# Kernel optimization log

Measured on AMD Instinct MI355X. Metric: run time of the kernel, lower is better.

The kernel has to match this reference:

```python
import jax, jax.numpy as jnp
import numpy as np

N, E, D, H, L, G, C = 50000, 800000, 128, 128, 3, 128, 10
BN_EPS = 1e-5


def setup_inputs() -> dict:
    key = jax.random.key(0)
    ks = jax.random.split(key, 16)
    inp = {
        "x": jax.random.normal(ks[0], (N, D), dtype=jnp.float32),
        "node_centrality": jax.random.uniform(ks[1], (N,), dtype=jnp.float32),
        "edge_centrality": jax.random.uniform(ks[2], (E,), dtype=jnp.float32),
        # stacked per-layer MLP params (in == hidden so stackable)
        "W1": jax.random.normal(ks[3], (L, D, H), dtype=jnp.float32) * 0.05,
        "b1": jnp.zeros((L, H), dtype=jnp.float32),
        "g1": jnp.ones((L, H), dtype=jnp.float32),
        "be1": jnp.zeros((L, H), dtype=jnp.float32),
        "W2": jax.random.normal(ks[4], (L, H, H), dtype=jnp.float32) * 0.05,
        "b2": jnp.zeros((L, H), dtype=jnp.float32),
        "Wc": jax.random.normal(ks[5], (H, C), dtype=jnp.float32) * 0.05,
        "bc": jnp.zeros((C,), dtype=jnp.float32),
        "edge_index": jax.random.randint(ks[6], (2, E), 0, N, dtype=jnp.int64),
        "batch": jnp.sort(jax.random.randint(ks[7], (N,), 0, G, dtype=jnp.int64)),
    }
    return inp


def _gin_forward(x, node_centrality, edge_centrality, W1, b1, g1, be1, W2, b2, Wc, bc, edge_index, batch):
    src, dst = edge_index[0], edge_index[1]  # x_j = x[src], aggregate at dst
    ec = edge_centrality[:, None]
    nc = node_centrality[:, None]
    for l in range(L):
        # message: gather + scale by edge centrality; aggr='add': scatter-add
        msg = x[src] * ec                                      # [E, H]
        agg = jax.ops.segment_sum(msg, dst, num_segments=N)    # [N, H]
        h = agg * nc + x                                       # (1 + eps) * x_r, eps = 0
        # MLP([in, hidden, hidden]): Linear -> BatchNorm(train) -> ReLU -> Linear
        h = h @ W1[l] + b1[l]
        mu = h.mean(axis=0)
        var = h.var(axis=0)  # biased, matches BN training stats
        h = (h - mu) * jax.lax.rsqrt(var + BN_EPS) * g1[l] + be1[l]
        h = jax.nn.relu(h)
        h = h @ W2[l] + b2[l]
        x = jax.nn.relu(h)  # outer .relu() in GIN.forward
    # global mean pool over graphs
    sums = jax.ops.segment_sum(x, batch, num_segments=G)           # [G, H]
    cnt = jax.ops.segment_sum(jnp.ones((N,), x.dtype), batch, num_segments=G)
    pooled = sums / jnp.maximum(cnt, 1.0)[:, None]
    return pooled @ Wc + bc  # [G, C]


def reference(x, edge_index, batch, node_centrality, edge_centrality, W1, b1, g1, be1, W2, b2, Wc, bc):
    return _gin_forward(x, node_centrality, edge_centrality, W1, b1, g1, be1, W2, b2, Wc, bc, edge_index, batch)
```

## Files before the change

### kernel.cpp

```cpp
#include <hip/hip_runtime.h>

#define Nn 50000
#define Ee 800000
#define HD 128
#define Ll 3
#define Gg 128
#define Cc 10
#define BN_EPS 1e-5f
#define NBLK1 782
#define PPAD 800
#define NSCB 49

__global__ void k_deg(const int* __restrict__ dst, int* __restrict__ deg) {
  int i = blockIdx.x * blockDim.x + threadIdx.x;
  int stride = gridDim.x * blockDim.x;
  for (int e = i; e < Ee; e += stride) atomicAdd(&deg[dst[e]], 1);
}

__global__ void k_scan1(const int* __restrict__ deg, int* __restrict__ offs,
                        int* __restrict__ bsum) {
  __shared__ int b0[1024], b1[1024];
  int tid = threadIdx.x;
  int i = blockIdx.x * 1024 + tid;
  int v = (i < Nn) ? deg[i] : 0;
  int* cur = b0; int* nxt = b1;
  cur[tid] = v;
  __syncthreads();
  for (int off = 1; off < 1024; off <<= 1) {
    int s = cur[tid] + ((tid >= off) ? cur[tid - off] : 0);
    nxt[tid] = s;
    __syncthreads();
    int* t = cur; cur = nxt; nxt = t;
  }
  if (i < Nn) offs[i] = cur[tid] - v;
  if (tid == 1023) bsum[blockIdx.x] = cur[1023];
}

__global__ void k_scan2(const int* __restrict__ bsum, int* __restrict__ carry) {
  int lane = threadIdx.x;
  int v = (lane < NSCB) ? bsum[lane] : 0;
  int s = v;
  for (int off = 1; off < 64; off <<= 1) {
    int t = __shfl_up(s, off, 64);
    if (lane >= off) s += t;
  }
  if (lane < NSCB) carry[lane] = s - v;
}

__global__ void k_scan3(const int* __restrict__ carry, int* __restrict__ offs,
                        int* __restrict__ cursor) {
  int i = blockIdx.x * 1024 + threadIdx.x;
  if (i < Nn) {
    int o = offs[i] + carry[blockIdx.x];
    offs[i] = o; cursor[i] = o;
  }
  if (i == 0) offs[Nn] = Ee;
}

__global__ void k_fill(const int* __restrict__ src, const int* __restrict__ dst,
                       const float* __restrict__ ec, int* __restrict__ cursor,
                       int* __restrict__ esrc, float* __restrict__ ew) {
  int i = blockIdx.x * blockDim.x + threadIdx.x;
  int stride = gridDim.x * blockDim.x;
  for (int e = i; e < Ee; e += stride) {
    int d = dst[e];
    int p = atomicAdd(&cursor[d], 1);
    esrc[p] = src[e];
    ew[p]   = ec[e];
  }
}

__global__ void k_agg(const float* __restrict__ xin, const int* __restrict__ offs,
                      const int* __restrict__ esrc, const float* __restrict__ ew,
                      float* __restrict__ agg) {
  int wid = threadIdx.x >> 6, lane = threadIdx.x & 63;
  int n = blockIdx.x * 4 + wid;
  if (n >= Nn) return;
  int beg = offs[n], end = offs[n + 1];
  const float2* x2 = (const float2*)xin;
  float2 acc0 = make_float2(0.f, 0.f);
  float2 acc1 = make_float2(0.f, 0.f);
  int j = beg;
  for (; j + 1 < end; j += 2) {
    int s0 = esrc[j], s1 = esrc[j + 1];
    float w0 = ew[j], w1 = ew[j + 1];
    float2 v0 = x2[s0 * 64 + lane];
    float2 v1 = x2[s1 * 64 + lane];
    acc0.x = fmaf(v0.x, w0, acc0.x); acc0.y = fmaf(v0.y, w0, acc0.y);
    acc1.x = fmaf(v1.x, w1, acc1.x); acc1.y = fmaf(v1.y, w1, acc1.y);
  }
  if (j < end) {
    int s0 = esrc[j];
    float w0 = ew[j];
    float2 v0 = x2[s0 * 64 + lane];
    acc0.x = fmaf(v0.x, w0, acc0.x); acc0.y = fmaf(v0.y, w0, acc0.y);
  }
  acc0.x += acc1.x; acc0.y += acc1.y;
  ((float2*)agg)[n * 64 + lane] = acc0;
}

__launch_bounds__(256, 2)
__global__ void k_gemm1(const float* __restrict__ agg, const float* __restrict__ nc,
                        const float* __restrict__ xin, const float* __restrict__ W,
                        const float* __restrict__ bias, float* __restrict__ out,
                        float* __restrict__ partial) {
  __shared__ float Als[64][132];
  __shared__ float4 Wls[64 * 32];
  int tid = threadIdx.x;
  int row0 = blockIdx.x * 64;

  int c4 = tid & 31, rr = tid >> 5;
  for (int it = 0; it < 8; ++it) {
    int r = rr + it * 8;
    int grow = row0 + r;
    float4 a = make_float4(0.f, 0.f, 0.f, 0.f);
    if (grow < Nn) {
      float4 ag = ((const float4*)agg)[grow * 32 + c4];
      float4 xv = ((const float4*)xin)[grow * 32 + c4];
      float nv = nc[grow];
      a.x = fmaf(ag.x, nv, xv.x); a.y = fmaf(ag.y, nv, xv.y);
      a.z = fmaf(ag.z, nv, xv.z); a.w = fmaf(ag.w, nv, xv.w);
    }
    *(float4*)&Als[r][c4 * 4] = a;
  }

  int tx = tid & 31, ty = tid >> 5;
  float acc[8][4];
#pragma unroll
  for (int i = 0; i < 8; ++i)
#pragma unroll
    for (int j = 0; j < 4; ++j) acc[i][j] = 0.f;

  for (int h = 0; h < 2; ++h) {
    if (h) __syncthreads();
    const float4* Wf4 = (const float4*)(W + h * 64 * 128);
    for (int i = tid; i < 2048; i += 256) Wls[i] = Wf4[i];
    __syncthreads();

#pragma unroll 4
    for (int kk = 0; kk < 64; kk += 4) {
      float4 b0 = Wls[(kk + 0) * 32 + tx];
      float4 b1v = Wls[(kk + 1) * 32 + tx];
      float4 b2v = Wls[(kk + 2) * 32 + tx];
      float4 b3v = Wls[(kk + 3) * 32 + tx];
#pragma unroll
      for (int i = 0; i < 8; ++i) {
        float4 av = *(const float4*)&Als[ty * 8 + i][h * 64 + kk];
        acc[i][0] = fmaf(av.x, b0.x, acc[i][0]); acc[i][1] = fmaf(av.x, b0.y, acc[i][1]);
        acc[i][2] = fmaf(av.x, b0.z, acc[i][2]); acc[i][3] = fmaf(av.x, b0.w, acc[i][3]);
        acc[i][0] = fmaf(av.y, b1v.x, acc[i][0]); acc[i][1] = fmaf(av.y, b1v.y, acc[i][1]);
        acc[i][2] = fmaf(av.y, b1v.z, acc[i][2]); acc[i][3] = fmaf(av.y, b1v.w, acc[i][3]);
        acc[i][0] = fmaf(av.z, b2v.x, acc[i][0]); acc[i][1] = fmaf(av.z, b2v.y, acc[i][1]);
        acc[i][2] = fmaf(av.z, b2v.z, acc[i][2]); acc[i][3] = fmaf(av.z, b2v.w, acc[i][3]);
        acc[i][0] = fmaf(av.w, b3v.x, acc[i][0]); acc[i][1] = fmaf(av.w, b3v.y, acc[i][1]);
        acc[i][2] = fmaf(av.w, b3v.z, acc[i][2]); acc[i][3] = fmaf(av.w, b3v.w, acc[i][3]);
      }
    }
  }

  float4 bcol = ((const float4*)bias)[tx];
  float s0 = 0, s1 = 0, s2 = 0, s3 = 0, q0 = 0, q1 = 0, q2 = 0, q3 = 0;
#pragma unroll
  for (int i = 0; i < 8; ++i) {
    int grow = row0 + ty * 8 + i;
    if (grow < Nn) {
      float4 o;
      o.x = acc[i][0] + bcol.x; o.y = acc[i][1] + bcol.y;
      o.z = acc[i][2] + bcol.z; o.w = acc[i][3] + bcol.w;
      ((float4*)out)[grow * 32 + tx] = o;
      s0 += o.x; s1 += o.y; s2 += o.z; s3 += o.w;
      q0 += o.x * o.x; q1 += o.y * o.y; q2 += o.z * o.z; q3 += o.w * o.w;
    }
  }

  __syncthreads();
  float* red = (float*)Als;
  red[tid * 8 + 0] = s0; red[tid * 8 + 1] = s1;
  red[tid * 8 + 2] = s2; red[tid * 8 + 3] = s3;
  red[tid * 8 + 4] = q0; red[tid * 8 + 5] = q1;
  red[tid * 8 + 6] = q2; red[tid * 8 + 7] = q3;
  __syncthreads();
  if (ty == 0) {
    float v[8];
#pragma unroll
    for (int j = 0; j < 8; ++j) v[j] = 0.f;
    for (int t = 0; t < 8; ++t) {
      int id = t * 32 + tx;
#pragma unroll
      for (int j = 0; j < 8; ++j) v[j] += red[id * 8 + j];
    }
    int blk = blockIdx.x;
#pragma unroll
    for (int j = 0; j < 4; ++j) {
      partial[(tx * 4 + j) * PPAD + blk]         = v[j];
      partial[(128 + tx * 4 + j) * PPAD + blk]   = v[4 + j];
    }
  }
}

__global__ void k_bnfin(const float* __restrict__ partial,
                        const float* __restrict__ g1, const float* __restrict__ be1,
                        float* __restrict__ scaleA, float* __restrict__ shiftA) {
  __shared__ float ss[256], qq[256];
  int f = blockIdx.x, t = threadIdx.x;
  float s = 0.f, q = 0.f;
  for (int b = t; b < NBLK1; b += 256) {
    s += partial[f * PPAD + b];
    q += partial[(128 + f) * PPAD + b];
  }
  ss[t] = s; qq[t] = q;
  __syncthreads();
  for (int off = 128; off > 0; off >>= 1) {
    if (t < off) { ss[t] += ss[t + off]; qq[t] += qq[t + off]; }
    __syncthreads();
  }
  if (t == 0) {
    const float inv = 1.0f / (float)Nn;
    float mu = ss[0] * inv;
    float var = fmaxf(qq[0] * inv - mu * mu, 0.f);
    float rs = rsqrtf(var + BN_EPS);
    float sc = rs * g1[f];
    scaleA[f] = sc;
    shiftA[f] = be1[f] - mu * sc;
  }
}

__launch_bounds__(256, 2)
__global__ void k_gemm2(const float* __restrict__ h1, const float* __restrict__ scaleA,
                        const float* __restrict__ shiftA, const float* __restrict__ W,
                        const float* __restrict__ bias, float* __restrict__ out) {
  __shared__ float Als[64][132];
  __shared__ float4 Wls[64 * 32];
  int tid = threadIdx.x;
  int row0 = blockIdx.x * 64;

  int c4 = tid & 31, rr = tid >> 5;
  float4 sc = ((const float4*)scaleA)[c4];
  float4 sh = ((const float4*)shiftA)[c4];
  for (int it = 0; it < 8; ++it) {
    int r = rr + it * 8;
    int grow = row0 + r;
    float4 a = make_float4(0.f, 0.f, 0.f, 0.f);
    if (grow < Nn) {
      float4 h = ((const float4*)h1)[grow * 32 + c4];
      a.x = fmaxf(fmaf(h.x, sc.x, sh.x), 0.f);
      a.y = fmaxf(fmaf(h.y, sc.y, sh.y), 0.f);
      a.z = fmaxf(fmaf(h.z, sc.z, sh.z), 0.f);
      a.w = fmaxf(fmaf(h.w, sc.w, sh.w), 0.f);
    }
    *(float4*)&Als[r][c4 * 4] = a;
  }

  int tx = tid & 31, ty = tid >> 5;
  float acc[8][4];
#pragma unroll
  for (int i = 0; i < 8; ++i)
#pragma unroll
    for (int j = 0; j < 4; ++j) acc[i][j] = 0.f;

  for (int h = 0; h < 2; ++h) {
    if (h) __syncthreads();
    const float4* Wf4 = (const float4*)(W + h * 64 * 128);
    for (int i = tid; i < 2048; i += 256) Wls[i] = Wf4[i];
    __syncthreads();

#pragma unroll 4
    for (int kk = 0; kk < 64; kk += 4) {
      float4 b0 = Wls[(kk + 0) * 32 + tx];
      float4 b1v = Wls[(kk + 1) * 32 + tx];
      float4 b2v = Wls[(kk + 2) * 32 + tx];
      float4 b3v = Wls[(kk + 3) * 32 + tx];
#pragma unroll
      for (int i = 0; i < 8; ++i) {
        float4 av = *(const float4*)&Als[ty * 8 + i][h * 64 + kk];
        acc[i][0] = fmaf(av.x, b0.x, acc[i][0]); acc[i][1] = fmaf(av.x, b0.y, acc[i][1]);
        acc[i][2] = fmaf(av.x, b0.z, acc[i][2]); acc[i][3] = fmaf(av.x, b0.w, acc[i][3]);
        acc[i][0] = fmaf(av.y, b1v.x, acc[i][0]); acc[i][1] = fmaf(av.y, b1v.y, acc[i][1]);
        acc[i][2] = fmaf(av.y, b1v.z, acc[i][2]); acc[i][3] = fmaf(av.y, b1v.w, acc[i][3]);
        acc[i][0] = fmaf(av.z, b2v.x, acc[i][0]); acc[i][1] = fmaf(av.z, b2v.y, acc[i][1]);
        acc[i][2] = fmaf(av.z, b2v.z, acc[i][2]); acc[i][3] = fmaf(av.z, b2v.w, acc[i][3]);
        acc[i][0] = fmaf(av.w, b3v.x, acc[i][0]); acc[i][1] = fmaf(av.w, b3v.y, acc[i][1]);
        acc[i][2] = fmaf(av.w, b3v.z, acc[i][2]); acc[i][3] = fmaf(av.w, b3v.w, acc[i][3]);
      }
    }
  }

  float4 bcol = ((const float4*)bias)[tx];
#pragma unroll
  for (int i = 0; i < 8; ++i) {
    int grow = row0 + ty * 8 + i;
    if (grow < Nn) {
      float4 o;
      o.x = fmaxf(acc[i][0] + bcol.x, 0.f);
      o.y = fmaxf(acc[i][1] + bcol.y, 0.f);
      o.z = fmaxf(acc[i][2] + bcol.z, 0.f);
      o.w = fmaxf(acc[i][3] + bcol.w, 0.f);
      ((float4*)out)[grow * 32 + tx] = o;
    }
  }
}

#define PCH 64
__global__ void k_pool(const float* __restrict__ xin, const int* __restrict__ batch,
                       float* __restrict__ pooled, float* __restrict__ gcnt) {
  int wid = threadIdx.x >> 6, lane = threadIdx.x & 63;
  int w = blockIdx.x * 4 + wid;
  int n0 = w * PCH;
  if (n0 >= Nn) return;
  int n1 = (n0 + PCH < Nn) ? n0 + PCH : Nn;
  const float2* x2 = (const float2*)xin;
  float2 acc = make_float2(0.f, 0.f);
  int cur = batch[n0];
  int cnt = 0;
  for (int n = n0; n < n1; ++n) {
    int g = batch[n];
    if (g != cur) {
      atomicAdd(&pooled[cur * 128 + lane * 2 + 0], acc.x);
      atomicAdd(&pooled[cur * 128 + lane * 2 + 1], acc.y);
      if (lane == 0) atomicAdd(&gcnt[cur], (float)cnt);
      acc = make_float2(0.f, 0.f); cnt = 0; cur = g;
    }
    float2 v = x2[n * 64 + lane];
    acc.x += v.x; acc.y += v.y; ++cnt;
  }
  atomicAdd(&pooled[cur * 128 + lane * 2 + 0], acc.x);
  atomicAdd(&pooled[cur * 128 + lane * 2 + 1], acc.y);
  if (lane == 0) atomicAdd(&gcnt[cur], (float)cnt);
}

__global__ void k_head(const float* __restrict__ pooled, const float* __restrict__ gcnt,
                       const float* __restrict__ Wc, const float* __restrict__ bc,
                       float* __restrict__ out) {
  __shared__ float p[128];
  int g = blockIdx.x, tid = threadIdx.x;
  p[tid] = pooled[g * 128 + tid] / fmaxf(gcnt[g], 1.0f);
  __syncthreads();
  if (tid < Cc) {
    float acc = bc[tid];
    for (int k = 0; k < 128; ++k) acc = fmaf(p[k], Wc[k * Cc + tid], acc);
    out[g * Cc + tid] = acc;
  }
}

extern "C" void kernel_launch(void* const* d_in, const int* in_sizes, int n_in,
                              void* d_out, int out_size, void* d_ws, size_t ws_size,
                              hipStream_t stream) {
  const float* x    = (const float*)d_in[0];
  const float* ncn  = (const float*)d_in[1];
  const float* ecn  = (const float*)d_in[2];
  const float* W1   = (const float*)d_in[3];
  const float* b1   = (const float*)d_in[4];
  const float* g1   = (const float*)d_in[5];
  const float* be1  = (const float*)d_in[6];
  const float* W2   = (const float*)d_in[7];
  const float* b2   = (const float*)d_in[8];
  const float* Wc   = (const float*)d_in[9];
  const float* bc   = (const float*)d_in[10];
  const int*   ei   = (const int*)d_in[11];
  const int*   batch= (const int*)d_in[12];
  const int* src  = ei;
  const int* dstp = ei + Ee;

  float* fws = (float*)d_ws;
  float* bufA     = fws;
  float* bufB     = fws +  6400000;
  float* h1       = fws + 12800000;
  float* partial  = fws + 19200000;
  float* scaleA   = partial + 256 * PPAD;
  float* shiftA   = scaleA + 128;
  float* pooled   = shiftA + 128;
  float* gcnt     = pooled + Gg * 128;
  int*   deg      = (int*)(gcnt + 128);
  int*   offs     = deg + Nn;
  int*   cursor   = offs + Nn + 64;
  int*   esrc     = cursor + Nn;
  float* ew       = (float*)(esrc + Ee);
  int*   bsum     = (int*)(ew + Ee);
  int*   carry    = bsum + 64;

  hipMemsetAsync(deg, 0, Nn * sizeof(int), stream);
  k_deg<<<1024, 256, 0, stream>>>(dstp, deg);
  k_scan1<<<NSCB, 1024, 0, stream>>>(deg, offs, bsum);
  k_scan2<<<1, 64, 0, stream>>>(bsum, carry);
  k_scan3<<<NSCB, 1024, 0, stream>>>(carry, offs, cursor);
  k_fill<<<1024, 256, 0, stream>>>(src, dstp, ecn, cursor, esrc, ew);

  const float* xin = x;
  for (int l = 0; l < Ll; ++l) {
    float* aggb = (l & 1) ? bufB : bufA;
    k_agg<<<(Nn + 3) / 4, 256, 0, stream>>>(xin, offs, esrc, ew, aggb);
    k_gemm1<<<NBLK1, 256, 0, stream>>>(aggb, ncn, xin, W1 + l * 128 * 128,
                                       b1 + l * 128, h1, partial);
    k_bnfin<<<128, 256, 0, stream>>>(partial, g1 + l * 128, be1 + l * 128,
                                     scaleA, shiftA);
    k_gemm2<<<NBLK1, 256, 0, stream>>>(h1, scaleA, shiftA, W2 + l * 128 * 128,
                                       b2 + l * 128, aggb);
    xin = aggb;
  }

  hipMemsetAsync(pooled, 0, (Gg * 128 + 128) * sizeof(float), stream);
  k_pool<<<(Nn + PCH * 4 - 1) / (PCH * 4), 256, 0, stream>>>(xin, batch, pooled, gcnt);
  k_head<<<Gg, 128, 0, stream>>>(pooled, gcnt, Wc, bc, (float*)d_out);
}
```

Measured before the change: 649.6 us.

## Use split-bf16 MFMA for the MLP GEMMs and pack the edge CSR arrays

Replaces the FP32 FMA shared-memory GEMMs with MFMA 16x16x32 bf16 instructions. Activations and weights are split into hi/lo bf16 pairs and three MFMAs are summed to recover near-FP32 accuracy. A new prep kernel transposes and splits W1/W2 once per call. Edge source and weight are packed into one int2 array, and the aggregation loop is unrolled to four edges to raise memory-level parallelism. The GEMMs now load A directly from global memory without LDS and use 128-thread blocks, which trades LDS reuse for MFMA throughput and adds a small approximation error.

```diff
diff --git a/kernel.cpp b/kernel.cpp
--- a/kernel.cpp
+++ b/kernel.cpp
@@ -10,6 +10,9 @@
 #define NBLK1 782
 #define PPAD 800
 #define NSCB 49
+
+typedef __attribute__((ext_vector_type(8))) __bf16 bf16x8;
+typedef __attribute__((ext_vector_type(4))) float f32x4;
 
 __global__ void k_deg(const int* __restrict__ dst, int* __restrict__ deg) {
   int i = blockIdx.x * blockDim.x + threadIdx.x;
@@ -59,141 +62,175 @@
 
 __global__ void k_fill(const int* __restrict__ src, const int* __restrict__ dst,
                        const float* __restrict__ ec, int* __restrict__ cursor,
-                       int* __restrict__ esrc, float* __restrict__ ew) {
+                       int2* __restrict__ epk) {
   int i = blockIdx.x * blockDim.x + threadIdx.x;
   int stride = gridDim.x * blockDim.x;
   for (int e = i; e < Ee; e += stride) {
     int d = dst[e];
     int p = atomicAdd(&cursor[d], 1);
-    esrc[p] = src[e];
-    ew[p]   = ec[e];
+    epk[p] = make_int2(src[e], __float_as_int(ec[e]));
+  }
+}
+
+__global__ void k_wprep(const float* __restrict__ W1, const float* __restrict__ W2,
+                        __bf16* __restrict__ wtHi, __bf16* __restrict__ wtLo) {
+  int mat = blockIdx.x >> 3;
+  int chunk = blockIdx.x & 7;
+  const float* W = (mat < 3) ? (W1 + mat * 16384) : (W2 + (mat - 3) * 16384);
+  __bf16* hi = wtHi + mat * 16384;
+  __bf16* lo = wtLo + mat * 16384;
+  for (int t = threadIdx.x; t < 2048; t += blockDim.x) {
+    int idx = chunk * 2048 + t;
+    int n = idx >> 7, k = idx & 127;
+    float v = W[k * 128 + n];
+    __bf16 h = (__bf16)v;
+    hi[idx] = h;
+    lo[idx] = (__bf16)(v - (float)h);
   }
 }
 
 __global__ void k_agg(const float* __restrict__ xin, const int* __restrict__ offs,
-                      const int* __restrict__ esrc, const float* __restrict__ ew,
-                      float* __restrict__ agg) {
+                      const int2* __restrict__ epk, float* __restrict__ agg) {
   int wid = threadIdx.x >> 6, lane = threadIdx.x & 63;
   int n = blockIdx.x * 4 + wid;
   if (n >= Nn) return;
   int beg = offs[n], end = offs[n + 1];
   const float2* x2 = (const float2*)xin;
-  float2 acc0 = make_float2(0.f, 0.f);
-  float2 acc1 = make_float2(0.f, 0.f);
+  float2 a0 = make_float2(0.f, 0.f), a1 = make_float2(0.f, 0.f);
+  float2 a2 = make_float2(0.f, 0.f), a3 = make_float2(0.f, 0.f);
   int j = beg;
-  for (; j + 1 < end; j += 2) {
-    int s0 = esrc[j], s1 = esrc[j + 1];
-    float w0 = ew[j], w1 = ew[j + 1];
-    float2 v0 = x2[s0 * 64 + lane];
-    float2 v1 = x2[s1 * 64 + lane];
-    acc0.x = fmaf(v0.x, w0, acc0.x); acc0.y = fmaf(v0.y, w0, acc0.y);
-    acc1.x = fmaf(v1.x, w1, acc1.x); acc1.y = fmaf(v1.y, w1, acc1.y);
-  }
-  if (j < end) {
-    int s0 = esrc[j];
-    float w0 = ew[j];
-    float2 v0 = x2[s0 * 64 + lane];
-    acc0.x = fmaf(v0.x, w0, acc0.x); acc0.y = fmaf(v0.y, w0, acc0.y);
-  }
-  acc0.x += acc1.x; acc0.y += acc1.y;
-  ((float2*)agg)[n * 64 + lane] = acc0;
-}
-
-__launch_bounds__(256, 2)
+  for (; j + 3 < end; j += 4) {
+    int2 e0 = epk[j], e1 = epk[j + 1], e2 = epk[j + 2], e3 = epk[j + 3];
+    float2 v0 = x2[e0.x * 64 + lane];
+    float2 v1 = x2[e1.x * 64 + lane];
+    float2 v2 = x2[e2.x * 64 + lane];
+    float2 v3 = x2[e3.x * 64 + lane];
+    float w0 = __int_as_float(e0.y), w1 = __int_as_float(e1.y);
+    float w2 = __int_as_float(e2.y), w3 = __int_as_float(e3.y);
+    a0.x = fmaf(v0.x, w0, a0.x); a0.y = fmaf(v0.y, w0, a0.y);
+    a1.x = fmaf(v1.x, w1, a1.x); a1.y = fmaf(v1.y, w1, a1.y);
+    a2.x = fmaf(v2.x, w2, a2.x); a2.y = fmaf(v2.y, w2, a2.y);
+    a3.x = fmaf(v3.x, w3, a3.x); a3.y = fmaf(v3.y, w3, a3.y);
+  }
+  for (; j < end; ++j) {
+    int2 e = epk[j];
+    float2 v = x2[e.x * 64 + lane];
+    float w = __int_as_float(e.y);
+    a0.x = fmaf(v.x, w, a0.x); a0.y = fmaf(v.y, w, a0.y);
+  }
+  a0.x += a1.x + a2.x + a3.x;
+  a0.y += a1.y + a2.y + a3.y;
+  ((float2*)agg)[n * 64 + lane] = a0;
+}
+
+__device__ __forceinline__ void split8(const float* a, bf16x8& hi, bf16x8& lo) {
+#pragma unroll
+  for (int j = 0; j < 8; ++j) {
+    float v = a[j];
+    __bf16 h = (__bf16)v;
+    hi[j] = h;
+    lo[j] = (__bf16)(v - (float)h);
+  }
+}
+
+__launch_bounds__(128)
 __global__ void k_gemm1(const float* __restrict__ agg, const float* __restrict__ nc,
-                        const float* __restrict__ xin, const float* __restrict__ W,
+                        const float* __restrict__ xin,
+                        const __bf16* __restrict__ wtHi, const __bf16* __restrict__ wtLo,
                         const float* __restrict__ bias, float* __restrict__ out,
                         float* __restrict__ partial) {
-  __shared__ float Als[64][132];
-  __shared__ float4 Wls[64 * 32];
   int tid = threadIdx.x;
+  int w = tid >> 6, l = tid & 63;
   int row0 = blockIdx.x * 64;
-
-  int c4 = tid & 31, rr = tid >> 5;
-  for (int it = 0; it < 8; ++it) {
-    int r = rr + it * 8;
-    int grow = row0 + r;
-    float4 a = make_float4(0.f, 0.f, 0.f, 0.f);
-    if (grow < Nn) {
-      float4 ag = ((const float4*)agg)[grow * 32 + c4];
-      float4 xv = ((const float4*)xin)[grow * 32 + c4];
-      float nv = nc[grow];
-      a.x = fmaf(ag.x, nv, xv.x); a.y = fmaf(ag.y, nv, xv.y);
-      a.z = fmaf(ag.z, nv, xv.z); a.w = fmaf(ag.w, nv, xv.w);
-    }
-    *(float4*)&Als[r][c4 * 4] = a;
-  }
-
-  int tx = tid & 31, ty = tid >> 5;
-  float acc[8][4];
-#pragma unroll
-  for (int i = 0; i < 8; ++i)
-#pragma unroll
-    for (int j = 0; j < 4; ++j) acc[i][j] = 0.f;
-
-  for (int h = 0; h < 2; ++h) {
-    if (h) __syncthreads();
-    const float4* Wf4 = (const float4*)(W + h * 64 * 128);
-    for (int i = tid; i < 2048; i += 256) Wls[i] = Wf4[i];
-    __syncthreads();
-
-#pragma unroll 4
-    for (int kk = 0; kk < 64; kk += 4) {
-      float4 b0 = Wls[(kk + 0) * 32 + tx];
-      float4 b1v = Wls[(kk + 1) * 32 + tx];
-      float4 b2v = Wls[(kk + 2) * 32 + tx];
-      float4 b3v = Wls[(kk + 3) * 32 + tx];
-#pragma unroll
-      for (int i = 0; i < 8; ++i) {
-        float4 av = *(const float4*)&Als[ty * 8 + i][h * 64 + kk];
-        acc[i][0] = fmaf(av.x, b0.x, acc[i][0]); acc[i][1] = fmaf(av.x, b0.y, acc[i][1]);
-        acc[i][2] = fmaf(av.x, b0.z, acc[i][2]); acc[i][3] = fmaf(av.x, b0.w, acc[i][3]);
-        acc[i][0] = fmaf(av.y, b1v.x, acc[i][0]); acc[i][1] = fmaf(av.y, b1v.y, acc[i][1]);
-        acc[i][2] = fmaf(av.y, b1v.z, acc[i][2]); acc[i][3] = fmaf(av.y, b1v.w, acc[i][3]);
-        acc[i][0] = fmaf(av.z, b2v.x, acc[i][0]); acc[i][1] = fmaf(av.z, b2v.y, acc[i][1]);
-        acc[i][2] = fmaf(av.z, b2v.z, acc[i][2]); acc[i][3] = fmaf(av.z, b2v.w, acc[i][3]);
-        acc[i][0] = fmaf(av.w, b3v.x, acc[i][0]); acc[i][1] = fmaf(av.w, b3v.y, acc[i][1]);
-        acc[i][2] = fmaf(av.w, b3v.z, acc[i][2]); acc[i][3] = fmaf(av.w, b3v.w, acc[i][3]);
-      }
-    }
-  }
-
-  float4 bcol = ((const float4*)bias)[tx];
-  float s0 = 0, s1 = 0, s2 = 0, s3 = 0, q0 = 0, q1 = 0, q2 = 0, q3 = 0;
-#pragma unroll
-  for (int i = 0; i < 8; ++i) {
-    int grow = row0 + ty * 8 + i;
-    if (grow < Nn) {
-      float4 o;
-      o.x = acc[i][0] + bcol.x; o.y = acc[i][1] + bcol.y;
-      o.z = acc[i][2] + bcol.z; o.w = acc[i][3] + bcol.w;
-      ((float4*)out)[grow * 32 + tx] = o;
-      s0 += o.x; s1 += o.y; s2 += o.z; s3 += o.w;
-      q0 += o.x * o.x; q1 += o.y * o.y; q2 += o.z * o.z; q3 += o.w * o.w;
-    }
-  }
-
-  __syncthreads();
-  float* red = (float*)Als;
-  red[tid * 8 + 0] = s0; red[tid * 8 + 1] = s1;
-  red[tid * 8 + 2] = s2; red[tid * 8 + 3] = s3;
-  red[tid * 8 + 4] = q0; red[tid * 8 + 5] = q1;
-  red[tid * 8 + 6] = q2; red[tid * 8 + 7] = q3;
-  __syncthreads();
-  if (ty == 0) {
-    float v[8];
-#pragma unroll
-    for (int j = 0; j < 8; ++j) v[j] = 0.f;
-    for (int t = 0; t < 8; ++t) {
-      int id = t * 32 + tx;
-#pragma unroll
-      for (int j = 0; j < 8; ++j) v[j] += red[id * 8 + j];
-    }
+  int l15 = l & 15, lg = l >> 4;
+  int colw = w * 64;
+  int krow = lg * 8;
+
+  f32x4 acc[4][4];
+#pragma unroll
+  for (int m = 0; m < 4; ++m)
+#pragma unroll
+    for (int n = 0; n < 4; ++n) acc[m][n] = (f32x4){0.f, 0.f, 0.f, 0.f};
+
+  int rowA[4]; bool rv[4]; float ncv[4];
+#pragma unroll
+  for (int m = 0; m < 4; ++m) {
+    rowA[m] = row0 + m * 16 + l15;
+    rv[m] = rowA[m] < Nn;
+    ncv[m] = rv[m] ? nc[rowA[m]] : 0.f;
+  }
+
+#pragma unroll
+  for (int ks = 0; ks < 4; ++ks) {
+    int k0 = ks * 32 + krow;
+    bf16x8 aHi[4], aLo[4];
+#pragma unroll
+    for (int m = 0; m < 4; ++m) {
+      float av[8];
+      if (rv[m]) {
+        const float* ap = agg + rowA[m] * 128 + k0;
+        const float* xp = xin + rowA[m] * 128 + k0;
+        f32x4 g0 = *(const f32x4*)ap, g1 = *(const f32x4*)(ap + 4);
+        f32x4 x0 = *(const f32x4*)xp, x1 = *(const f32x4*)(xp + 4);
+#pragma unroll
+        for (int jj = 0; jj < 4; ++jj) {
+          av[jj]     = fmaf(g0[jj], ncv[m], x0[jj]);
+          av[4 + jj] = fmaf(g1[jj], ncv[m], x1[jj]);
+        }
+      } else {
+#pragma unroll
+        for (int jj = 0; jj < 8; ++jj) av[jj] = 0.f;
+      }
+      split8(av, aHi[m], aLo[m]);
+    }
+    bf16x8 bHi[4], bLo[4];
+#pragma unroll
+    for (int n = 0; n < 4; ++n) {
+      int c = colw + n * 16 + l15;
+      bHi[n] = *(const bf16x8*)(wtHi + c * 128 + k0);
+      bLo[n] = *(const bf16x8*)(wtLo + c * 128 + k0);
+    }
+#pragma unroll
+    for (int m = 0; m < 4; ++m)
+#pragma unroll
+      for (int n = 0; n < 4; ++n) {
+        acc[m][n] = __builtin_amdgcn_mfma_f32_16x16x32_bf16(aHi[m], bHi[n], acc[m][n], 0, 0, 0);
+        acc[m][n] = __builtin_amdgcn_mfma_f32_16x16x32_bf16(aLo[m], bHi[n], acc[m][n], 0, 0, 0);
+        acc[m][n] = __builtin_amdgcn_mfma_f32_16x16x32_bf16(aHi[m], bLo[n], acc[m][n], 0, 0, 0);
+      }
+  }
+
+  float s[4] = {0.f, 0.f, 0.f, 0.f}, q[4] = {0.f, 0.f, 0.f, 0.f};
+#pragma unroll
+  for (int n = 0; n < 4; ++n) {
+    int c = colw + n * 16 + l15;
+    float bv = bias[c];
+#pragma unroll
+    for (int m = 0; m < 4; ++m) {
+      int rbase = row0 + m * 16 + lg * 4;
+#pragma unroll
+      for (int r = 0; r < 4; ++r) {
+        int rr = rbase + r;
+        if (rr < Nn) {
+          float o = acc[m][n][r] + bv;
+          out[rr * 128 + c] = o;
+          s[n] += o; q[n] += o * o;
+        }
+      }
+    }
+  }
+#pragma unroll
+  for (int n = 0; n < 4; ++n) {
+    s[n] += __shfl_xor(s[n], 16, 64); q[n] += __shfl_xor(q[n], 16, 64);
+    s[n] += __shfl_xor(s[n], 32, 64); q[n] += __shfl_xor(q[n], 32, 64);
+  }
+  if (lg == 0) {
     int blk = blockIdx.x;
 #pragma unroll
-    for (int j = 0; j < 4; ++j) {
-      partial[(tx * 4 + j) * PPAD + blk]         = v[j];
-      partial[(128 + tx * 4 + j) * PPAD + blk]   = v[4 + j];
+    for (int n = 0; n < 4; ++n) {
+      int f = colw + n * 16 + l15;
+      partial[f * PPAD + blk] = s[n];
+      partial[(128 + f) * PPAD + blk] = q[n];
     }
   }
 }
@@ -225,77 +262,83 @@
   }
 }
 
-__launch_bounds__(256, 2)
+__launch_bounds__(128)
 __global__ void k_gemm2(const float* __restrict__ h1, const float* __restrict__ scaleA,
-                        const float* __restrict__ shiftA, const float* __restrict__ W,
+                        const float* __restrict__ shiftA,
+                        const __bf16* __restrict__ wtHi, const __bf16* __restrict__ wtLo,
                         const float* __restrict__ bias, float* __restrict__ out) {
-  __shared__ float Als[64][132];
-  __shared__ float4 Wls[64 * 32];
   int tid = threadIdx.x;
+  int w = tid >> 6, l = tid & 63;
   int row0 = blockIdx.x * 64;
-
-  int c4 = tid & 31, rr = tid >> 5;
-  float4 sc = ((const float4*)scaleA)[c4];
-  float4 sh = ((const float4*)shiftA)[c4];
-  for (int it = 0; it < 8; ++it) {
-    int r = rr + it * 8;
-    int grow = row0 + r;
-    float4 a = make_float4(0.f, 0.f, 0.f, 0.f);
-    if (grow < Nn) {
-      float4 h = ((const float4*)h1)[grow * 32 + c4];
-      a.x = fmaxf(fmaf(h.x, sc.x, sh.x), 0.f);
-      a.y = fmaxf(fmaf(h.y, sc.y, sh.y), 0.f);
-      a.z = fmaxf(fmaf(h.z, sc.z, sh.z), 0.f);
-      a.w = fmaxf(fmaf(h.w, sc.w, sh.w), 0.f);
-    }
-    *(float4*)&Als[r][c4 * 4] = a;
-  }
-
-  int tx = tid & 31, ty = tid >> 5;
-  float acc[8][4];
-#pragma unroll
-  for (int i = 0; i < 8; ++i)
-#pragma unroll
-    for (int j = 0; j < 4; ++j) acc[i][j] = 0.f;
-
-  for (int h = 0; h < 2; ++h) {
-    if (h) __syncthreads();
-    const float4* Wf4 = (const float4*)(W + h * 64 * 128);
-    for (int i = tid; i < 2048; i += 256) Wls[i] = Wf4[i];
-    __syncthreads();
-
-#pragma unroll 4
-    for (int kk = 0; kk < 64; kk += 4) {
-      float4 b0 = Wls[(kk + 0) * 32 + tx];
-      float4 b1v = Wls[(kk + 1) * 32 + tx];
-      float4 b2v = Wls[(kk + 2) * 32 + tx];
-      float4 b3v = Wls[(kk + 3) * 32 + tx];
-#pragma unroll
-      for (int i = 0; i < 8; ++i) {
-        float4 av = *(const float4*)&Als[ty * 8 + i][h * 64 + kk];
-        acc[i][0] = fmaf(av.x, b0.x, acc[i][0]); acc[i][1] = fmaf(av.x, b0.y, acc[i][1]);
-        acc[i][2] = fmaf(av.x, b0.z, acc[i][2]); acc[i][3] = fmaf(av.x, b0.w, acc[i][3]);
-        acc[i][0] = fmaf(av.y, b1v.x, acc[i][0]); acc[i][1] = fmaf(av.y, b1v.y, acc[i][1]);
-        acc[i][2] = fmaf(av.y, b1v.z, acc[i][2]); acc[i][3] = fmaf(av.y, b1v.w, acc[i][3]);
-        acc[i][0] = fmaf(av.z, b2v.x, acc[i][0]); acc[i][1] = fmaf(av.z, b2v.y, acc[i][1]);
-        acc[i][2] = fmaf(av.z, b2v.z, acc[i][2]); acc[i][3] = fmaf(av.z, b2v.w, acc[i][3]);
-        acc[i][0] = fmaf(av.w, b3v.x, acc[i][0]); acc[i][1] = fmaf(av.w, b3v.y, acc[i][1]);
-        acc[i][2] = fmaf(av.w, b3v.z, acc[i][2]); acc[i][3] = fmaf(av.w, b3v.w, acc[i][3]);
-      }
-    }
-  }
-
-  float4 bcol = ((const float4*)bias)[tx];
-#pragma unroll
-  for (int i = 0; i < 8; ++i) {
-    int grow = row0 + ty * 8 + i;
-    if (grow < Nn) {
-      float4 o;
-      o.x = fmaxf(acc[i][0] + bcol.x, 0.f);
-      o.y = fmaxf(acc[i][1] + bcol.y, 0.f);
-      o.z = fmaxf(acc[i][2] + bcol.z, 0.f);
-      o.w = fmaxf(acc[i][3] + bcol.w, 0.f);
-      ((float4*)out)[grow * 32 + tx] = o;
+  int l15 = l & 15, lg = l >> 4;
+  int colw = w * 64;
+  int krow = lg * 8;
+
+  f32x4 acc[4][4];
+#pragma unroll
+  for (int m = 0; m < 4; ++m)
+#pragma unroll
+    for (int n = 0; n < 4; ++n) acc[m][n] = (f32x4){0.f, 0.f, 0.f, 0.f};
+
+  int rowA[4]; bool rv[4];
+#pragma unroll
+  for (int m = 0; m < 4; ++m) {
+    rowA[m] = row0 + m * 16 + l15;
+    rv[m] = rowA[m] < Nn;
+  }
+
+#pragma unroll
+  for (int ks = 0; ks < 4; ++ks) {
+    int k0 = ks * 32 + krow;
+    f32x4 sc0 = *(const f32x4*)(scaleA + k0), sc1 = *(const f32x4*)(scaleA + k0 + 4);
+    f32x4 sh0 = *(const f32x4*)(shiftA + k0), sh1 = *(const f32x4*)(shiftA + k0 + 4);
+    bf16x8 aHi[4], aLo[4];
+#pragma unroll
+    for (int m = 0; m < 4; ++m) {
+      float av[8];
+      if (rv[m]) {
+        const float* hp = h1 + rowA[m] * 128 + k0;
+        f32x4 h0 = *(const f32x4*)hp, h1v = *(const f32x4*)(hp + 4);
+#pragma unroll
+        for (int jj = 0; jj < 4; ++jj) {
+          av[jj]     = fmaxf(fmaf(h0[jj],  sc0[jj], sh0[jj]), 0.f);
+          av[4 + jj] = fmaxf(fmaf(h1v[jj], sc1[jj], sh1[jj]), 0.f);
+        }
+      } else {
+#pragma unroll
+        for (int jj = 0; jj < 8; ++jj) av[jj] = 0.f;
+      }
+      split8(av, aHi[m], aLo[m]);
+    }
+    bf16x8 bHi[4], bLo[4];
+#pragma unroll
+    for (int n = 0; n < 4; ++n) {
+      int c = colw + n * 16 + l15;
+      bHi[n] = *(const bf16x8*)(wtHi + c * 128 + k0);
+      bLo[n] = *(const bf16x8*)(wtLo + c * 128 + k0);
+    }
+#pragma unroll
+    for (int m = 0; m < 4; ++m)
+#pragma unroll
+      for (int n = 0; n < 4; ++n) {
+        acc[m][n] = __builtin_amdgcn_mfma_f32_16x16x32_bf16(aHi[m], bHi[n], acc[m][n], 0, 0, 0);
+        acc[m][n] = __builtin_amdgcn_mfma_f32_16x16x32_bf16(aLo[m], bHi[n], acc[m][n], 0, 0, 0);
+        acc[m][n] = __builtin_amdgcn_mfma_f32_16x16x32_bf16(aHi[m], bLo[n], acc[m][n], 0, 0, 0);
+      }
+  }
+
+#pragma unroll
+  for (int n = 0; n < 4; ++n) {
+    int c = colw + n * 16 + l15;
+    float bv = bias[c];
+#pragma unroll
+    for (int m = 0; m < 4; ++m) {
+      int rbase = row0 + m * 16 + lg * 4;
+#pragma unroll
+      for (int r = 0; r < 4; ++r) {
+        int rr = rbase + r;
+        if (rr < Nn) out[rr * 128 + c] = fmaxf(acc[m][n][r] + bv, 0.f);
+      }
     }
   }
 }
@@ -370,30 +413,35 @@
   float* shiftA   = scaleA + 128;
   float* pooled   = shiftA + 128;
   float* gcnt     = pooled + Gg * 128;
-  int*   deg      = (int*)(gcnt + 128);
+  int*   ib       = (int*)(gcnt + 128);
+  int*   deg      = ib;
   int*   offs     = deg + Nn;
   int*   cursor   = offs + Nn + 64;
-  int*   esrc     = cursor + Nn;
-  float* ew       = (float*)(esrc + Ee);
-  int*   bsum     = (int*)(ew + Ee);
+  int*   bsum     = cursor + Nn;
   int*   carry    = bsum + 64;
-
+  int2*  epk      = (int2*)(carry + 64);
+  __bf16* wtHi    = (__bf16*)(epk + Ee);
+  __bf16* wtLo    = wtHi + 6 * 16384;
+
+  k_wprep<<<48, 256, 0, stream>>>(W1, W2, wtHi, wtLo);
   hipMemsetAsync(deg, 0, Nn * sizeof(int), stream);
   k_deg<<<1024, 256, 0, stream>>>(dstp, deg);
   k_scan1<<<NSCB, 1024, 0, stream>>>(deg, offs, bsum);
   k_scan2<<<1, 64, 0, stream>>>(bsum, carry);
   k_scan3<<<NSCB, 1024, 0, stream>>>(carry, offs, cursor);
-  k_fill<<<1024, 256, 0, stream>>>(src, dstp, ecn, cursor, esrc, ew);
+  k_fill<<<1024, 256, 0, stream>>>(src, dstp, ecn, cursor, epk);
 
   const float* xin = x;
   for (int l = 0; l < Ll; ++l) {
     float* aggb = (l & 1) ? bufB : bufA;
-    k_agg<<<(Nn + 3) / 4, 256, 0, stream>>>(xin, offs, esrc, ew, aggb);
-    k_gemm1<<<NBLK1, 256, 0, stream>>>(aggb, ncn, xin, W1 + l * 128 * 128,
+    k_agg<<<(Nn + 3) / 4, 256, 0, stream>>>(xin, offs, epk, aggb);
+    k_gemm1<<<NBLK1, 128, 0, stream>>>(aggb, ncn, xin,
+                                       wtHi + l * 16384, wtLo + l * 16384,
                                        b1 + l * 128, h1, partial);
     k_bnfin<<<128, 256, 0, stream>>>(partial, g1 + l * 128, be1 + l * 128,
                                      scaleA, shiftA);
-    k_gemm2<<<NBLK1, 256, 0, stream>>>(h1, scaleA, shiftA, W2 + l * 128 * 128,
+    k_gemm2<<<NBLK1, 128, 0, stream>>>(h1, scaleA, shiftA,
+                                       wtHi + (3 + l) * 16384, wtLo + (3 + l) * 16384,
                                        b2 + l * 128, aggb);
     xin = aggb;
   }
```

Result: faster. 583.9 us (-10.1%).
